# Optimization experiments

Measured on AMD Instinct MI355X. Metric: run time of the kernel, lower is better.

## Reference

```python
import jax, jax.numpy as jnp
import numpy as np

B, NV, CIN, C = 1, 40000, 128, 64
D, H, W = 19, 200, 176  # sparse_shape = output_shape[1:4] + [1,0,0]
EPS = 1e-3
DN = ('NCDHW', 'OIDHW', 'NCDHW')


def setup_inputs():
    key = jax.random.key(0)
    ks = jax.random.split(key, 12)
    vf = jax.random.normal(ks[0], (NV, CIN), jnp.float32)
    bi = jnp.zeros((NV, 1), jnp.int32)
    zi = jax.random.randint(ks[1], (NV, 1), 0, D, jnp.int32)
    yi = jax.random.randint(ks[2], (NV, 1), 0, H, jnp.int32)
    xi = jax.random.randint(ks[3], (NV, 1), 0, W, jnp.int32)
    coors = jnp.concatenate([bi, zi, yi, xi], axis=1)  # [batch, z, y, x]
    s = 0.05
    w_sub1 = jax.random.normal(ks[4], (C, CIN, 3, 3, 3), jnp.float32) * s
    w_down1 = jax.random.normal(ks[5], (C, C, 3, 1, 1), jnp.float32) * s
    w_sub2 = jax.random.normal(ks[6], (C, C, 3, 3, 3), jnp.float32) * s
    w_sub3 = jax.random.normal(ks[7], (C, C, 3, 3, 3), jnp.float32) * s
    w_down2 = jax.random.normal(ks[8], (C, C, 3, 1, 1), jnp.float32) * s
    bn_gamma = 1.0 + 0.1 * jax.random.normal(ks[9], (5, C), jnp.float32)
    bn_beta = 0.1 * jax.random.normal(ks[10], (5, C), jnp.float32)
    bn_mean = 0.1 * jax.random.normal(ks[11], (5, C), jnp.float32)
    bn_var = jnp.ones((5, C), jnp.float32)
    return dict(voxel_features=vf, coors=coors, batch_size=1,
                w_sub1=w_sub1, w_down1=w_down1, w_sub2=w_sub2, w_sub3=w_sub3,
                w_down2=w_down2, bn_gamma=bn_gamma, bn_beta=bn_beta,
                bn_mean=bn_mean, bn_var=bn_var)


def _conv(x, w, stride, pad):
    return jax.lax.conv_general_dilated(x, w, stride, pad, dimension_numbers=DN)


def _bnrelu(x, i, mask, g, b, m, v):
    # eval-mode BN on active sites only (inactive sites stay exactly zero -> mask)
    inv = jax.lax.rsqrt(v[i] + EPS)
    y = (x - m[i][None, :, None, None, None]) * (g[i] * inv)[None, :, None, None, None] \
        + b[i][None, :, None, None, None]
    return jnp.maximum(y, 0.0) * mask


def _forward(voxel_features, coors, batch_size, w_sub1, w_down1, w_sub2, w_sub3,
             w_down2, bn_gamma, bn_beta, bn_mean, bn_var):
    bi, zi, yi, xi = coors[:, 0], coors[:, 1], coors[:, 2], coors[:, 3]
    # scn.InputLayer: scatter (sum duplicates) active voxel features into dense grid
    dense = jnp.zeros((batch_size, D, H, W, CIN), voxel_features.dtype)
    dense = dense.at[bi, zi, yi, xi].add(voxel_features)
    x = jnp.transpose(dense, (0, 4, 1, 2, 3))  # NCDHW
    mask = jnp.zeros((batch_size, D, H, W), voxel_features.dtype)
    mask = mask.at[bi, zi, yi, xi].set(1.0)[:, None]  # [B,1,D,H,W] active sites
    ones_k = jnp.ones((1, 1, 3, 1, 1), x.dtype)
    pad1 = ((1, 1), (1, 1), (1, 1))
    bn = (bn_gamma, bn_beta, bn_mean, bn_var)
    # SubmanifoldConvolution(128->64, k3) + BNReLU : output only at active sites
    x = _bnrelu(_conv(x, w_sub1, (1, 1, 1), pad1) * mask, 0, mask, *bn)
    # Convolution 64->64 kernel (3,1,1) stride (2,1,1): new active set = any input in window
    x = _conv(x, w_down1, (2, 1, 1), 'VALID')
    mask = (_conv(mask, ones_k, (2, 1, 1), 'VALID') > 0).astype(x.dtype)
    x = _bnrelu(x, 1, mask, *bn)
    # two more submanifold convs
    x = _bnrelu(_conv(x, w_sub2, (1, 1, 1), pad1) * mask, 2, mask, *bn)
    x = _bnrelu(_conv(x, w_sub3, (1, 1, 1), pad1) * mask, 3, mask, *bn)
    # second strided conv
    x = _conv(x, w_down2, (2, 1, 1), 'VALID')
    mask = (_conv(mask, ones_k, (2, 1, 1), 'VALID') > 0).astype(x.dtype)
    x = _bnrelu(x, 4, mask, *bn)
    # SparseToDense then view(N, C*D, H, W)
    Nb, Cc, Dd, Hh, Ww = x.shape
    return x.reshape(Nb, Cc * Dd, Hh, Ww)


def reference(voxel_features, coors, batch_size, w_sub1, w_down1, w_sub2, w_sub3,
              w_down2, bn_gamma, bn_beta, bn_mean, bn_var):
    return _forward(voxel_features, coors, batch_size, w_sub1, w_down1, w_sub2,
                    w_sub3, w_down2, bn_gamma, bn_beta, bn_mean, bn_var)
```

## Files before the change

kernel.cpp:

```cpp
#include <hip/hip_runtime.h>

typedef float floatx4 __attribute__((ext_vector_type(4)));
typedef _Float16 f16x8 __attribute__((ext_vector_type(8)));

#define D0_ 19
#define H0_ 200
#define W0_ 176
#define HW_ (H0_*W0_)
#define NCELL0 (D0_*HW_)
#define D1_ 9
#define NCELL1 (D1_*HW_)
#define D2_ 4
#define NCELL2 (D2_*HW_)
#define NV_ 40000
#define CAP0 40000
#define CAP1 80000
#define CAP2 140800
#define EPS_ 1e-3f

typedef __attribute__((address_space(1))) const unsigned int* gas_t;
typedef __attribute__((address_space(3))) unsigned int* las_t;

__device__ __forceinline__ short f2h(float f){
    _Float16 h = (_Float16)f;
    short s; __builtin_memcpy(&s, &h, 2); return s;
}

__device__ __forceinline__ void repack_one(const float* w, short* Bout, int i,
                                           int KCsrc, int kshift, int NSP){
    int k = i >> 6, n = i & 63;
    int j = k >> kshift;
    int ci = k & (KCsrc - 1);
    short val = f2h(w[(n * KCsrc + ci) * NSP + j]);
    int chunk = k >> 5, lanehi = (k >> 3) & 3, jj = k & 7;
    int nt = n >> 4, lane = lanehi * 16 + (n & 15);
    Bout[((chunk * 4 + nt) * 64 + lane) * 8 + jj] = val;
}

#define RP1 (3456*64)
#define RP2 (1728*64)
#define RPD (192*64)

__global__ void k_prep(const float* w1, const float* w2, const float* w3,
                       const float* wd1, const float* wd2,
                       short* B1, short* B2, short* B3, short* Bd1, short* Bd2,
                       const float* g, const float* b, const float* m, const float* v,
                       float* scale, float* shift,
                       const int* coors, int* cntg){
    int i = blockIdx.x * 256 + threadIdx.x;
    if (i < RP1){ repack_one(w1, B1, i, 128, 7, 27); return; }
    i -= RP1;
    if (i < RP2){ repack_one(w2, B2, i, 64, 6, 27); return; }
    i -= RP2;
    if (i < RP2){ repack_one(w3, B3, i, 64, 6, 27); return; }
    i -= RP2;
    if (i < RPD){ repack_one(wd1, Bd1, i, 64, 6, 3); return; }
    i -= RPD;
    if (i < RPD){ repack_one(wd2, Bd2, i, 64, 6, 3); return; }
    i -= RPD;
    if (i < 5*64){
        float s = g[i] / sqrtf(v[i] + EPS_);
        scale[i] = s;
        shift[i] = b[i] - m[i] * s;
        return;
    }
    i -= 5*64;
    if (i < NV_){
        int z = coors[i*4+1], y = coors[i*4+2], x = coors[i*4+3];
        atomicAdd(&cntg[(z*H0_ + y)*W0_ + x], 1);
    }
}
#define PREP_TOT (RP1 + 2*RP2 + 2*RPD + 5*64 + NV_)

__device__ __forceinline__ int blk_rank(bool act, int* cnt, int& r_out){
    unsigned long long mask = __ballot(act);
    int lane = threadIdx.x & 63, wid = threadIdx.x >> 6;
    int wrank = __popcll(mask & ((1ull << lane) - 1));
    __shared__ int ws[4];
    __shared__ int blkbase;
    if (lane == 0) ws[wid] = __popcll(mask);
    __syncthreads();
    if (threadIdx.x == 0){
        int t0 = ws[0], t1 = ws[1], t2 = ws[2], t3 = ws[3];
        int tot = t0 + t1 + t2 + t3;
        blkbase = tot ? atomicAdd(cnt, tot) : 0;
        ws[0] = 0; ws[1] = t0; ws[2] = t0 + t1; ws[3] = t0 + t1 + t2;
    }
    __syncthreads();
    r_out = blkbase + ws[wid] + wrank;
    return 0;
}

__global__ void k_compact0(const int* cntg, int* idx0, int* list0, int* cnt0){
    int c = blockIdx.x * 256 + threadIdx.x;
    bool act = (c < NCELL0) && (cntg[c] > 0);
    int r; blk_rank(act, cnt0, r);
    if (c >= NCELL0) return;
    if (act){
        idx0[c] = r;
        int z = c / HW_; int rem = c - z * HW_;
        int y = rem / W0_; int x = rem - y * W0_;
        list0[r] = (z << 16) | (y << 8) | x;
    } else idx0[c] = -1;
}

__global__ void k_compact_dn(const int* idxsrc, int* idxdst, int* listdst, int* cnt,
                             int ncell){
    int c = blockIdx.x * 256 + threadIdx.x;
    bool act = false;
    int d = 0, y = 0, x = 0;
    if (c < ncell){
        d = c / HW_; int rem = c - d * HW_;
        y = rem / W0_; x = rem - y * W0_;
        #pragma unroll
        for (int j = 0; j < 3; ++j)
            act = act || (idxsrc[((2*d + j)*H0_ + y)*W0_ + x] >= 0);
    }
    int r; blk_rank(act, cnt, r);
    if (c >= ncell) return;
    if (act){
        idxdst[c] = r;
        listdst[r] = (d << 16) | (y << 8) | x;
    } else idxdst[c] = -1;
}

__global__ void k_scatter(const float* vf, const int* coors, const int* cntg,
                          const int* idx0, float* feat0f){
    int u = blockIdx.x * 256 + threadIdx.x;
    if (u >= NV_ * 32) return;
    int v = u >> 5, c4 = u & 31;
    int z = coors[v*4+1], y = coors[v*4+2], x = coors[v*4+3];
    int cell = (z*H0_ + y)*W0_ + x;
    int row = idx0[cell];
    float4 s = ((const float4*)(vf + (long)v * 128))[c4];
    float* dst = feat0f + (long)row * 128 + c4 * 4;
    if (cntg[cell] == 1){
        *(float4*)dst = s;
    } else {
        atomicAdd(dst+0, s.x); atomicAdd(dst+1, s.y);
        atomicAdd(dst+2, s.z); atomicAdd(dst+3, s.w);
    }
}

__global__ void k_convert(const float* f, short* b, const int* cntp){
    int n8 = cntp[0] * 16;
    int i = blockIdx.x * 256 + threadIdx.x;
    if (i >= n8) return;
    float4 a = ((const float4*)f)[i*2], c = ((const float4*)f)[i*2+1];
    short o[8] = { f2h(a.x), f2h(a.y), f2h(a.z), f2h(a.w),
                   f2h(c.x), f2h(c.y), f2h(c.z), f2h(c.w) };
    ((int4*)b)[i] = *(int4*)o;
}

template<int NCH>
__global__ __launch_bounds__(256) void k_gemm27(
    const short* __restrict__ featA, const int* __restrict__ list,
    const int* __restrict__ idxg, int Dd,
    const short* __restrict__ Bs, short* __restrict__ out,
    const int* __restrict__ cntp,
    const float* __restrict__ scale, const float* __restrict__ shift)
{
    __shared__ short Blds[2][NCH*4*512];
    constexpr int NT = 27;
    const int ROWS = NCH * 32;
    int M = *cntp;
    int m0 = blockIdx.x * 64;
    if (m0 >= M) return;
    int tid = threadIdx.x;
    int wave = tid >> 6, lane = tid & 63;
    int m16 = lane & 15;
    int koff = (lane >> 4) * 8;

    int row = m0 + wave * 16 + m16;
    bool ok = row < M;
    int cell = ok ? list[row] : 0xFF0000;
    int z = cell >> 16, y = (cell >> 8) & 255, x = cell & 255;

    floatx4 acc[4] = {};
    f16x8 A[3][NCH];
    const f16x8 z8 = {0,0,0,0,0,0,0,0};

    auto stageB = [&](int j, int b){
        #pragma unroll
        for (int f = 0; f < NCH; ++f){
            int frag = wave * NCH + f;
            const short* g = Bs + (((long)j * NCH * 4 + frag) * 64 + lane) * 8;
            __builtin_amdgcn_global_load_lds((gas_t)g, (las_t)&Blds[b][frag * 512],
                                             16, 0, 0);
        }
    };
    auto getR = [&](int t)->int{
        int nz = z + t/9 - 1, ny = y + (t/3)%3 - 1, nx = x + t%3 - 1;
        int r = -1;
        if ((unsigned)nz < (unsigned)Dd && (unsigned)ny < H0_ && (unsigned)nx < W0_)
            r = idxg[(nz*H0_ + ny)*W0_ + nx];
        return r;
    };
    auto loadA = [&](f16x8* dst, int r){
        #pragma unroll
        for (int kc = 0; kc < NCH; ++kc)
            dst[kc] = (r >= 0) ? *(const f16x8*)(featA + (long)r*ROWS + koff + kc*32) : z8;
    };

    int r0 = getR(0), r1 = getR(1), r2 = getR(2);
    stageB(0, 0);
    loadA(A[0], r0);
    loadA(A[1], r1);
    __syncthreads();

    #pragma unroll
    for (int t = 0; t < NT; ++t){
        if (t + 1 < NT) stageB(t + 1, (t + 1) & 1);
        if (t + 2 < NT) loadA(A[(t + 2) % 3], r2);
        int rn = (t + 3 < NT) ? getR(t + 3) : -1;
        if (__ballot(r0 >= 0) != 0){
            const short* Bb = Blds[t & 1];
            #pragma unroll
            for (int kc = 0; kc < NCH; ++kc){
                f16x8 b[4];
                #pragma unroll
                for (int nt = 0; nt < 4; ++nt)
                    b[nt] = *(const f16x8*)&Bb[((kc*4 + nt) * 64 + lane) * 8];
                f16x8 a = A[t % 3][kc];
                #pragma unroll
                for (int nt = 0; nt < 4; ++nt)
                    acc[nt] = __builtin_amdgcn_mfma_f32_16x16x32_f16(a, b[nt], acc[nt], 0, 0, 0);
            }
        }
        r0 = r1; r1 = r2; r2 = rn;
        __syncthreads();
    }

    int n16 = lane & 15;
    int mb = m0 + wave * 16 + (lane >> 4) * 4;
    #pragma unroll
    for (int nt = 0; nt < 4; ++nt){
        int n = nt * 16 + n16;
        float sc = scale[n], sh = shift[n];
        #pragma unroll
        for (int r = 0; r < 4; ++r){
            int site = mb + r;
            if (site < M)
                out[(long)site*64 + n] = f2h(fmaxf(acc[nt][r] * sc + sh, 0.f));
        }
    }
}

template<bool FINAL>
__global__ __launch_bounds__(256) void k_gemmdn(
    const short* __restrict__ featA, const int* __restrict__ list,
    const int* __restrict__ idxg, int parentD,
    const short* __restrict__ Bs, short* __restrict__ out,
    const int* __restrict__ cntp,
    const float* __restrict__ scale, const float* __restrict__ shift,
    float* __restrict__ dout)
{
    __shared__ short Blds[2][2*4*512];
    constexpr int NT = 3;
    const int ROWS = 64;
    int M = *cntp;
    int m0 = blockIdx.x * 64;
    if (m0 >= M) return;
    int tid = threadIdx.x;
    int wave = tid >> 6, lane = tid & 63;
    int m16 = lane & 15;
    int koff = (lane >> 4) * 8;

    int row = m0 + wave * 16 + m16;
    bool ok = row < M;
    int cell = ok ? list[row] : 0;
    int d = ok ? (cell >> 16) : 300;
    int y = (cell >> 8) & 255, x = cell & 255;

    floatx4 acc[4] = {};
    f16x8 A[3][2];
    const f16x8 z8 = {0,0,0,0,0,0,0,0};

    auto stageB = [&](int j, int b){
        #pragma unroll
        for (int f = 0; f < 2; ++f){
            int frag = wave * 2 + f;
            const short* g = Bs + (((long)j * 8 + frag) * 64 + lane) * 8;
            __builtin_amdgcn_global_load_lds((gas_t)g, (las_t)&Blds[b][frag * 512],
                                             16, 0, 0);
        }
    };
    auto getR = [&](int t)->int{
        int pz = 2*d + t;
        int r = -1;
        if ((unsigned)pz < (unsigned)parentD)
            r = idxg[(pz*H0_ + y)*W0_ + x];
        return r;
    };
    auto loadA = [&](f16x8* dst, int r){
        #pragma unroll
        for (int kc = 0; kc < 2; ++kc)
            dst[kc] = (r >= 0) ? *(const f16x8*)(featA + (long)r*ROWS + koff + kc*32) : z8;
    };

    int r0 = getR(0), r1 = getR(1), r2 = getR(2);
    stageB(0, 0);
    loadA(A[0], r0);
    loadA(A[1], r1);
    __syncthreads();

    #pragma unroll
    for (int t = 0; t < NT; ++t){
        if (t + 1 < NT) stageB(t + 1, (t + 1) & 1);
        if (t + 2 < NT) loadA(A[(t + 2) % 3], r2);
        if (__ballot(r0 >= 0) != 0){
            const short* Bb = Blds[t & 1];
            #pragma unroll
            for (int kc = 0; kc < 2; ++kc){
                f16x8 b[4];
                #pragma unroll
                for (int nt = 0; nt < 4; ++nt)
                    b[nt] = *(const f16x8*)&Bb[((kc*4 + nt) * 64 + lane) * 8];
                f16x8 a = A[t % 3][kc];
                #pragma unroll
                for (int nt = 0; nt < 4; ++nt)
                    acc[nt] = __builtin_amdgcn_mfma_f32_16x16x32_f16(a, b[nt], acc[nt], 0, 0, 0);
            }
        }
        r0 = r1; r1 = r2; r2 = -1;
        __syncthreads();
    }

    int n16 = lane & 15;
    int mb = m0 + wave * 16 + (lane >> 4) * 4;
    #pragma unroll
    for (int nt = 0; nt < 4; ++nt){
        int n = nt * 16 + n16;
        float sc = scale[n], sh = shift[n];
        #pragma unroll
        for (int r = 0; r < 4; ++r){
            int site = mb + r;
            if (site < M){
                float yv = fmaxf(acc[nt][r] * sc + sh, 0.f);
                if (FINAL){
                    int c2 = list[site];
                    int dd = c2 >> 16, yy = (c2 >> 8) & 255, xx = c2 & 255;
                    dout[((n*4 + dd)*H0_ + yy)*W0_ + xx] = yv;
                } else {
                    out[(long)site*64 + n] = f2h(yv);
                }
            }
        }
    }
}

extern "C" void kernel_launch(void* const* d_in, const int* in_sizes, int n_in,
                              void* d_out, int out_size, void* d_ws, size_t ws_size,
                              hipStream_t stream){
    const float* vf   = (const float*)d_in[0];
    const int*   coors= (const int*)  d_in[1];
    const float* w1   = (const float*)d_in[3];
    const float* wd1  = (const float*)d_in[4];
    const float* w2   = (const float*)d_in[5];
    const float* w3   = (const float*)d_in[6];
    const float* wd2  = (const float*)d_in[7];
    const float* bng  = (const float*)d_in[8];
    const float* bnb  = (const float*)d_in[9];
    const float* bnm  = (const float*)d_in[10];
    const float* bnv  = (const float*)d_in[11];
    float* dout = (float*)d_out;

    char* ws = (char*)d_ws;
    size_t off = 0;
    auto alloc = [&](size_t bytes)->char* {
        char* p = ws + off;
        off += (bytes + 255) & ~(size_t)255;
        return p;
    };

    int*   counters = (int*)  alloc(256);
    int*   cntg     = (int*)  alloc((size_t)NCELL0 * 4);
    int*   idx0     = (int*)  alloc((size_t)NCELL0 * 4);
    int*   idx1     = (int*)  alloc((size_t)NCELL1 * 4);
    int*   idx2     = (int*)  alloc((size_t)NCELL2 * 4);
    int*   list0    = (int*)  alloc((size_t)CAP0 * 4);
    int*   list1    = (int*)  alloc((size_t)CAP1 * 4);
    int*   list2    = (int*)  alloc((size_t)CAP2 * 4);
    float* feat0f   = (float*)alloc((size_t)CAP0 * 128 * 4);
    short* feat0h   = (short*)alloc((size_t)CAP0 * 128 * 2);
    short* feat1    = (short*)alloc((size_t)CAP0 * 64 * 2);
    short* featd1   = (short*)alloc((size_t)CAP1 * 64 * 2);
    short* feat2    = (short*)alloc((size_t)CAP1 * 64 * 2);
    short* feat3    = (short*)alloc((size_t)CAP1 * 64 * 2);
    short* B1  = (short*)alloc((size_t)3456 * 64 * 2);
    short* B2  = (short*)alloc((size_t)1728 * 64 * 2);
    short* B3  = (short*)alloc((size_t)1728 * 64 * 2);
    short* Bd1 = (short*)alloc((size_t)192 * 64 * 2);
    short* Bd2 = (short*)alloc((size_t)192 * 64 * 2);
    float* bnscale = (float*)alloc(5 * 64 * 4);
    float* bnshift = (float*)alloc(5 * 64 * 4);

    hipMemsetAsync(counters, 0, 256 + (size_t)NCELL0 * 4, stream);
    hipMemsetAsync(feat0f, 0, (size_t)CAP0 * 128 * 4, stream);
    hipMemsetAsync(dout, 0, (size_t)out_size * 4, stream);

    k_prep<<<(PREP_TOT + 255)/256, 256, 0, stream>>>(w1, w2, w3, wd1, wd2,
        B1, B2, B3, Bd1, Bd2, bng, bnb, bnm, bnv, bnscale, bnshift, coors, cntg);

    k_compact0<<<(NCELL0 + 255)/256, 256, 0, stream>>>(cntg, idx0, list0, counters + 0);
    k_scatter<<<(NV_*32 + 255)/256, 256, 0, stream>>>(vf, coors, cntg, idx0, feat0f);
    k_convert<<<(CAP0*16 + 255)/256, 256, 0, stream>>>(feat0f, feat0h, counters + 0);
    k_compact_dn<<<(NCELL1 + 255)/256, 256, 0, stream>>>(idx0, idx1, list1, counters + 1, NCELL1);
    k_compact_dn<<<(NCELL2 + 255)/256, 256, 0, stream>>>(idx1, idx2, list2, counters + 2, NCELL2);

    k_gemm27<4><<<(CAP0+63)/64, 256, 0, stream>>>(feat0h, list0, idx0, D0_, B1, feat1,
        counters + 0, bnscale + 0,   bnshift + 0);
    k_gemmdn<false><<<(CAP1+63)/64, 256, 0, stream>>>(feat1, list1, idx0, D0_, Bd1, featd1,
        counters + 1, bnscale + 64,  bnshift + 64,  nullptr);
    k_gemm27<2><<<(CAP1+63)/64, 256, 0, stream>>>(featd1, list1, idx1, D1_, B2, feat2,
        counters + 1, bnscale + 128, bnshift + 128);
    k_gemm27<2><<<(CAP1+63)/64, 256, 0, stream>>>(feat2, list1, idx1, D1_, B3, feat3,
        counters + 1, bnscale + 192, bnshift + 192);
    k_gemmdn<true><<<(CAP2+63)/64, 256, 0, stream>>>(feat3, list2, idx1, D1_, Bd2, nullptr,
        counters + 2, bnscale + 256, bnshift + 256, dout);
}
```

Before: 288.9 us.

## Batch kernel taps per pipeline stage and zero only duplicate-voxel rows

The 27-tap gather GEMM now processes TB taps per pipeline stage. Each stage stages TB taps of weights into LDS, which cuts the number of barriers and staging rounds for the 64-channel subconvs (TB=2). The full memset of the fp32 scatter buffer is removed. In its place, compact0 zeroes only the rows of cells with more than one voxel, since single-voxel cells are written directly. The trade-off is more registers for A fragments and a larger LDS footprint, which may reduce occupancy.

```diff
diff --git a/kernel.cpp b/kernel.cpp
--- a/kernel.cpp
+++ b/kernel.cpp
@@ -91,7 +91,8 @@
     return 0;
 }
 
-__global__ void k_compact0(const int* cntg, int* idx0, int* list0, int* cnt0){
+__global__ void k_compact0(const int* cntg, int* idx0, int* list0, int* cnt0,
+                           float* feat0f){
     int c = blockIdx.x * 256 + threadIdx.x;
     bool act = (c < NCELL0) && (cntg[c] > 0);
     int r; blk_rank(act, cnt0, r);
@@ -101,6 +102,12 @@
         int z = c / HW_; int rem = c - z * HW_;
         int y = rem / W0_; int x = rem - y * W0_;
         list0[r] = (z << 16) | (y << 8) | x;
+        if (cntg[c] > 1){
+            float4 zz = {0,0,0,0};
+            float4* p = (float4*)(feat0f + (long)r * 128);
+            #pragma unroll
+            for (int i = 0; i < 32; ++i) p[i] = zz;
+        }
     } else idx0[c] = -1;
 }
 
@@ -152,7 +159,7 @@
     ((int4*)b)[i] = *(int4*)o;
 }
 
-template<int NCH>
+template<int NCH, int TB>
 __global__ __launch_bounds__(256) void k_gemm27(
     const short* __restrict__ featA, const int* __restrict__ list,
     const int* __restrict__ idxg, int Dd,
@@ -160,8 +167,11 @@
     const int* __restrict__ cntp,
     const float* __restrict__ scale, const float* __restrict__ shift)
 {
-    __shared__ short Blds[2][NCH*4*512];
     constexpr int NT = 27;
+    constexpr int NS = (NT + TB - 1) / TB;
+    constexpr int FPS = TB * NCH * 4;
+    constexpr int FPW = TB * NCH;
+    __shared__ short Blds[2][FPS * 512];
     const int ROWS = NCH * 32;
     int M = *cntp;
     int m0 = blockIdx.x * 64;
@@ -177,19 +187,21 @@
     int z = cell >> 16, y = (cell >> 8) & 255, x = cell & 255;
 
     floatx4 acc[4] = {};
-    f16x8 A[3][NCH];
+    f16x8 A[3][TB][NCH];
+    int rr[3][TB];
     const f16x8 z8 = {0,0,0,0,0,0,0,0};
 
-    auto stageB = [&](int j, int b){
-        #pragma unroll
-        for (int f = 0; f < NCH; ++f){
-            int frag = wave * NCH + f;
-            const short* g = Bs + (((long)j * NCH * 4 + frag) * 64 + lane) * 8;
-            __builtin_amdgcn_global_load_lds((gas_t)g, (las_t)&Blds[b][frag * 512],
+    auto stageB = [&](int s, int b){
+        #pragma unroll
+        for (int f = 0; f < FPW; ++f){
+            int L = wave * FPW + f;
+            const short* g = Bs + ((long)s * FPS + L) * 512 + (long)lane * 8;
+            __builtin_amdgcn_global_load_lds((gas_t)g, (las_t)&Blds[b][L * 512],
                                              16, 0, 0);
         }
     };
     auto getR = [&](int t)->int{
+        if (t >= NT) return -1;
         int nz = z + t/9 - 1, ny = y + (t/3)%3 - 1, nx = x + t%3 - 1;
         int r = -1;
         if ((unsigned)nz < (unsigned)Dd && (unsigned)ny < H0_ && (unsigned)nx < W0_)
@@ -202,32 +214,50 @@
             dst[kc] = (r >= 0) ? *(const f16x8*)(featA + (long)r*ROWS + koff + kc*32) : z8;
     };
 
-    int r0 = getR(0), r1 = getR(1), r2 = getR(2);
+    #pragma unroll
+    for (int k = 0; k < 3; ++k)
+        #pragma unroll
+        for (int j = 0; j < TB; ++j)
+            rr[k][j] = getR(k*TB + j);
     stageB(0, 0);
-    loadA(A[0], r0);
-    loadA(A[1], r1);
+    #pragma unroll
+    for (int k = 0; k < 2; ++k)
+        #pragma unroll
+        for (int j = 0; j < TB; ++j)
+            loadA(A[k][j], rr[k][j]);
     __syncthreads();
 
     #pragma unroll
-    for (int t = 0; t < NT; ++t){
-        if (t + 1 < NT) stageB(t + 1, (t + 1) & 1);
-        if (t + 2 < NT) loadA(A[(t + 2) % 3], r2);
-        int rn = (t + 3 < NT) ? getR(t + 3) : -1;
-        if (__ballot(r0 >= 0) != 0){
-            const short* Bb = Blds[t & 1];
+    for (int s = 0; s < NS; ++s){
+        if (s + 1 < NS) stageB(s + 1, (s + 1) & 1);
+        if (s + 2 < NS){
             #pragma unroll
-            for (int kc = 0; kc < NCH; ++kc){
-                f16x8 b[4];
+            for (int j = 0; j < TB; ++j)
+                loadA(A[(s+2)%3][j], rr[(s+2)%3][j]);
+        }
+        int rn[TB];
+        #pragma unroll
+        for (int j = 0; j < TB; ++j)
+            rn[j] = getR((s+3)*TB + j);
+        const short* Bb = Blds[s & 1];
+        #pragma unroll
+        for (int j = 0; j < TB; ++j){
+            if (s*TB + j < NT && __ballot(rr[s%3][j] >= 0) != 0){
                 #pragma unroll
-                for (int nt = 0; nt < 4; ++nt)
-                    b[nt] = *(const f16x8*)&Bb[((kc*4 + nt) * 64 + lane) * 8];
-                f16x8 a = A[t % 3][kc];
-                #pragma unroll
-                for (int nt = 0; nt < 4; ++nt)
-                    acc[nt] = __builtin_amdgcn_mfma_f32_16x16x32_f16(a, b[nt], acc[nt], 0, 0, 0);
+                for (int kc = 0; kc < NCH; ++kc){
+                    f16x8 b[4];
+                    #pragma unroll
+                    for (int nt = 0; nt < 4; ++nt)
+                        b[nt] = *(const f16x8*)&Bb[(((j*NCH + kc)*4 + nt) * 512) + lane * 8];
+                    f16x8 a = A[s%3][j][kc];
+                    #pragma unroll
+                    for (int nt = 0; nt < 4; ++nt)
+                        acc[nt] = __builtin_amdgcn_mfma_f32_16x16x32_f16(a, b[nt], acc[nt], 0, 0, 0);
+                }
             }
         }
-        r0 = r1; r1 = r2; r2 = rn;
+        #pragma unroll
+        for (int j = 0; j < TB; ++j) rr[s%3][j] = rn[j];
         __syncthreads();
     }
 
@@ -396,25 +426,24 @@
     float* bnshift = (float*)alloc(5 * 64 * 4);
 
     hipMemsetAsync(counters, 0, 256 + (size_t)NCELL0 * 4, stream);
-    hipMemsetAsync(feat0f, 0, (size_t)CAP0 * 128 * 4, stream);
     hipMemsetAsync(dout, 0, (size_t)out_size * 4, stream);
 
     k_prep<<<(PREP_TOT + 255)/256, 256, 0, stream>>>(w1, w2, w3, wd1, wd2,
         B1, B2, B3, Bd1, Bd2, bng, bnb, bnm, bnv, bnscale, bnshift, coors, cntg);
 
-    k_compact0<<<(NCELL0 + 255)/256, 256, 0, stream>>>(cntg, idx0, list0, counters + 0);
+    k_compact0<<<(NCELL0 + 255)/256, 256, 0, stream>>>(cntg, idx0, list0, counters + 0, feat0f);
     k_scatter<<<(NV_*32 + 255)/256, 256, 0, stream>>>(vf, coors, cntg, idx0, feat0f);
     k_convert<<<(CAP0*16 + 255)/256, 256, 0, stream>>>(feat0f, feat0h, counters + 0);
     k_compact_dn<<<(NCELL1 + 255)/256, 256, 0, stream>>>(idx0, idx1, list1, counters + 1, NCELL1);
     k_compact_dn<<<(NCELL2 + 255)/256, 256, 0, stream>>>(idx1, idx2, list2, counters + 2, NCELL2);
 
-    k_gemm27<4><<<(CAP0+63)/64, 256, 0, stream>>>(feat0h, list0, idx0, D0_, B1, feat1,
+    k_gemm27<4,1><<<(CAP0+63)/64, 256, 0, stream>>>(feat0h, list0, idx0, D0_, B1, feat1,
         counters + 0, bnscale + 0,   bnshift + 0);
     k_gemmdn<false><<<(CAP1+63)/64, 256, 0, stream>>>(feat1, list1, idx0, D0_, Bd1, featd1,
         counters + 1, bnscale + 64,  bnshift + 64,  nullptr);
-    k_gemm27<2><<<(CAP1+63)/64, 256, 0, stream>>>(featd1, list1, idx1, D1_, B2, feat2,
+    k_gemm27<2,2><<<(CAP1+63)/64, 256, 0, stream>>>(featd1, list1, idx1, D1_, B2, feat2,
         counters + 1, bnscale + 128, bnshift + 128);
-    k_gemm27<2><<<(CAP1+63)/64, 256, 0, stream>>>(feat2, list1, idx1, D1_, B3, feat3,
+    k_gemm27<2,2><<<(CAP1+63)/64, 256, 0, stream>>>(feat2, list1, idx1, D1_, B3, feat3,
         counters + 1, bnscale + 192, bnshift + 192);
     k_gemmdn<true><<<(CAP2+63)/64, 256, 0, stream>>>(feat3, list2, idx1, D1_, Bd2, nullptr,
         counters + 2, bnscale + 256, bnshift + 256, dout);
```

Result: no change. 289.2 us (+0.1%).
